# Optimization experiments

Hardware: AMD Instinct MI355X
Metric: run time of the kernel (lower is better)

Reference implementation:

```python
import jax, jax.numpy as jnp
import numpy as np

H = 16          # nhead
N_LAYERS = 4    # stacks (weights are SHARED across stacks, as in the torch module)
PAD_IDX = 1
EPS = 1e-6
NEG = -1e9


def _pos_encoding(S, d):
    den = jnp.exp(-jnp.arange(0, d, 2, dtype=jnp.float32) * (np.log(10000.0) / d))
    ang = jnp.arange(S, dtype=jnp.float32)[:, None] * den[None, :]  # (S, d/2)
    pe = jnp.zeros((S, d), jnp.float32)
    pe = pe.at[:, 0::2].set(jnp.sin(ang)).at[:, 1::2].set(jnp.cos(ang))
    return pe


def _layer_norm(x, g, b):
    mu = jnp.mean(x, axis=-1, keepdims=True)
    var = jnp.mean((x - mu) ** 2, axis=-1, keepdims=True)
    return (x - mu) * jax.lax.rsqrt(var + EPS) * g + b


def _split_heads(x):
    B, S, d = x.shape
    return x.reshape(B, S, H, d // H).transpose(0, 2, 1, 3)  # (B,H,S,dk)


def _mha(q_in, k_in, v_in, mask, wq, bq, wk, bk, wv, bv, wo, bo):
    q = _split_heads(q_in @ wq + bq)
    k = _split_heads(k_in @ wk + bk)
    v = _split_heads(v_in @ wv + bv)
    dk = v.shape[-1]
    score = jnp.einsum('bhqd,bhkd->bhqk', q, k) / jnp.sqrt(jnp.float32(dk))
    if mask is not None:
        score = jnp.where(mask, score, NEG)
    p = jax.nn.softmax(score, axis=-1)
    out = jnp.einsum('bhqk,bhkd->bhqd', p, v)
    B, _, S, _ = out.shape
    out = out.transpose(0, 2, 1, 3).reshape(B, S, H * dk)
    return out @ wo + bo


def setup_inputs() -> dict:
    key = jax.random.key(0)
    B, St, Sm, d, dff, V = 4, 1024, 1024, 1024, 4096, 32000
    ks = jax.random.split(key, 32)
    sc = 1.0 / np.sqrt(d)
    inp = {
        'target_result': jax.random.randint(ks[0], (B, St), 0, V),
        'memory': jax.random.normal(ks[1], (B, Sm, d), jnp.float32),
        'emb': jax.random.normal(ks[2], (V, d), jnp.float32) * sc,
        'ff_w1': jax.random.normal(ks[3], (d, dff), jnp.float32) * sc,
        'ff_b1': jnp.zeros((dff,), jnp.float32),
        'ff_w2': jax.random.normal(ks[4], (dff, d), jnp.float32) / np.sqrt(dff),
        'ff_b2': jnp.zeros((d,), jnp.float32),
        'ln_g': jnp.ones((d,), jnp.float32),
        'ln_b': jnp.zeros((d,), jnp.float32),
    }
    i = 5
    for pre in ('sa', 'xa'):
        for nm in ('q', 'k', 'v', 'o'):
            inp[f'{pre}_w{nm}'] = jax.random.normal(ks[i], (d, d), jnp.float32) * sc
            inp[f'{pre}_b{nm}'] = jnp.zeros((d,), jnp.float32)
            i += 1
    return inp


def reference(target_result, memory, emb,
              sa_wq, sa_bq, sa_wk, sa_bk, sa_wv, sa_bv, sa_wo, sa_bo,
              xa_wq, xa_bq, xa_wk, xa_bk, xa_wv, xa_bv, xa_wo, xa_bo,
              ff_w1, ff_b1, ff_w2, ff_b2, ln_g, ln_b):
    B, St = target_result.shape
    d = emb.shape[1]
    # embed + scale + positional encoding (dropout = eval/identity)
    x = emb[target_result] * jnp.sqrt(jnp.float32(d)) + _pos_encoding(St, d)[None]
    # masks: pad mask (B,1,St,1) & causal (St,St) -> (B,1,St,St); source mask all-ones -> None
    pad = (target_result != PAD_IDX)[:, None, :, None]
    causal = jnp.tril(jnp.ones((St, St), bool))[None, None]
    tgt_mask = pad & causal
    out = x
    for _ in range(N_LAYERS):
        n = _layer_norm(out, ln_g, ln_b)
        out = out + _mha(n, n, n, tgt_mask,
                         sa_wq, sa_bq, sa_wk, sa_bk, sa_wv, sa_bv, sa_wo, sa_bo)
        n = _layer_norm(out, ln_g, ln_b)
        out = out + _mha(n, memory, memory, None,
                         xa_wq, xa_bq, xa_wk, xa_bk, xa_wv, xa_bv, xa_wo, xa_bo)
        n = _layer_norm(out, ln_g, ln_b)
        out = out + (jax.nn.relu(n @ ff_w1 + ff_b1) @ ff_w2 + ff_b2)
    return _layer_norm(out, ln_g, ln_b)
```

## Files before the change

### kernel.cpp

```cpp
#include <hip/hip_runtime.h>

typedef unsigned short u16;
typedef unsigned int u32;
typedef float f32x4 __attribute__((ext_vector_type(4)));
typedef float f32x16 __attribute__((ext_vector_type(16)));
typedef __bf16 bf16x8 __attribute__((ext_vector_type(8)));
typedef short short8 __attribute__((ext_vector_type(8)));
typedef u32 u32x4 __attribute__((ext_vector_type(4)));

#define DINLINE static __device__ __forceinline__

DINLINE u16 f2bf(float f) {
  u32 u = __builtin_bit_cast(u32, f);
  u += 0x7fffu + ((u >> 16) & 1u);
  return (u16)(u >> 16);
}

DINLINE float b2f(u32 lo16) {
  u32 u = lo16 << 16;
  return __builtin_bit_cast(float, u);
}

DINLINE f32x4 mfma16(short8 a, short8 b, f32x4 c) {
  return __builtin_amdgcn_mfma_f32_16x16x32_bf16(
      __builtin_bit_cast(bf16x8, a), __builtin_bit_cast(bf16x8, b), c, 0, 0, 0);
}

DINLINE f32x16 mfma32(short8 a, short8 b, f32x16 c) {
  return __builtin_amdgcn_mfma_f32_32x32x16_bf16(
      __builtin_bit_cast(bf16x8, a), __builtin_bit_cast(bf16x8, b), c, 0, 0, 0);
}

DINLINE u32 cvtpk(float lo, float hi) {
  u32 r;
  asm("v_cvt_pk_bf16_f32 %0, %1, %2" : "=v"(r) : "v"(lo), "v"(hi));
  return r;
}

DINLINE void plswap(u32& a, u32& b) {
  auto r = __builtin_amdgcn_permlane32_swap(a, b, false, false);
  a = (u32)r[0];
  b = (u32)r[1];
}

DINLINE void gld16(const void* g, void* l) {
  __builtin_amdgcn_global_load_lds(
      (const __attribute__((address_space(1))) void*)g,
      (__attribute__((address_space(3))) void*)l, 16, 0, 0);
}

struct W8 {
  const float* src[8];
  u16* dst[8];
  float scale[8];
};
__global__ __launch_bounds__(256) void transpose_wt8(W8 p) {
  __shared__ float tile[32][33];
  const int z = blockIdx.z;
  const float* __restrict__ src = p.src[z];
  u16* __restrict__ dst = p.dst[z];
  const float scale = p.scale[z];
  int n0 = blockIdx.x * 32, k0 = blockIdx.y * 32;
  int tx = threadIdx.x, ty = threadIdx.y;
#pragma unroll
  for (int j = 0; j < 32; j += 8)
    tile[ty + j][tx] = src[(size_t)(k0 + ty + j) * 1024 + n0 + tx];
  __syncthreads();
#pragma unroll
  for (int j = 0; j < 32; j += 8)
    dst[(size_t)(n0 + ty + j) * 1024 + k0 + tx] = f2bf(tile[tx][ty + j] * scale);
}

__global__ __launch_bounds__(256) void transpose_wt(const float* __restrict__ src,
                                                    u16* __restrict__ dst, int K, int N,
                                                    float scale) {
  __shared__ float tile[32][33];
  int n0 = blockIdx.x * 32, k0 = blockIdx.y * 32;
  int tx = threadIdx.x, ty = threadIdx.y;
#pragma unroll
  for (int j = 0; j < 32; j += 8)
    tile[ty + j][tx] = src[(size_t)(k0 + ty + j) * N + n0 + tx];
  __syncthreads();
#pragma unroll
  for (int j = 0; j < 32; j += 8)
    dst[(size_t)(n0 + ty + j) * K + k0 + tx] = f2bf(tile[tx][ty + j] * scale);
}

__global__ __launch_bounds__(256) void cvt_bf16(const float* __restrict__ src,
                                                u16* __restrict__ dst) {
  size_t i = (size_t)blockIdx.x * 256 + threadIdx.x;
  float4 v = ((const float4*)src)[i];
  u32 lo = (u32)f2bf(v.x) | ((u32)f2bf(v.y) << 16);
  u32 hi = (u32)f2bf(v.z) | ((u32)f2bf(v.w) << 16);
  uint2 o; o.x = lo; o.y = hi;
  ((uint2*)dst)[i] = o;
}

__global__ void prep_bias(const float* __restrict__ a, const float* __restrict__ b,
                          const float* __restrict__ c, const float* __restrict__ xq,
                          float* __restrict__ oqkv, float* __restrict__ oxq, float sa) {
  int i = blockIdx.x * 256 + threadIdx.x;
  if (i < 1024) oqkv[i] = a[i] * sa;
  else if (i < 2048) oqkv[i] = b[i - 1024];
  else if (i < 3072) oqkv[i] = c[i - 2048];
  else oxq[i - 3072] = xq[i - 3072] * sa;
}

__global__ __launch_bounds__(256) void pe_k(float* __restrict__ pe) {
  int s = blockIdx.x;
  for (int c = threadIdx.x; c < 1024; c += 256) {
    int i = c >> 1;
    float den = expf(-(float)(2 * i) * 0.0089944739960705f);
    float ang = (float)s * den;
    pe[s * 1024 + c] = (c & 1) ? cosf(ang) : sinf(ang);
  }
}

__global__ __launch_bounds__(256) void embed_pe(const int* __restrict__ tgt,
                                                const float* __restrict__ emb,
                                                const float* __restrict__ pe,
                                                float* __restrict__ x,
                                                u16* __restrict__ xbf) {
  int row = blockIdx.x;
  int s = row & 1023;
  int tok = tgt[row];
  float4 e = ((const float4*)(emb + (size_t)tok * 1024))[threadIdx.x];
  float4 p = ((const float4*)(pe + (size_t)s * 1024))[threadIdx.x];
  float4 o;
  o.x = e.x * 32.0f + p.x; o.y = e.y * 32.0f + p.y;
  o.z = e.z * 32.0f + p.z; o.w = e.w * 32.0f + p.w;
  ((float4*)(x + (size_t)row * 1024))[threadIdx.x] = o;
  ushort4 ob;
  ob.x = f2bf(o.x); ob.y = f2bf(o.y); ob.z = f2bf(o.z); ob.w = f2bf(o.w);
  ((ushort4*)(xbf + (size_t)row * 1024))[threadIdx.x] = ob;
}

template <int MODE>
__global__ __launch_bounds__(256) void ln2_k(const float* __restrict__ Xf,
                                             const u16* __restrict__ Xb,
                                             const float* __restrict__ g,
                                             const float* __restrict__ bta,
                                             u16* __restrict__ obf,
                                             float* __restrict__ of) {
  const int t = threadIdx.x;
  const int row = blockIdx.x * 2 + (t >> 7);
  const int c = t & 127;
  float v[8];
  if (MODE == 1) {
    float4 a = ((const float4*)(Xf + (size_t)row * 1024))[c * 2];
    float4 b4 = ((const float4*)(Xf + (size_t)row * 1024))[c * 2 + 1];
    v[0] = a.x; v[1] = a.y; v[2] = a.z; v[3] = a.w;
    v[4] = b4.x; v[5] = b4.y; v[6] = b4.z; v[7] = b4.w;
  } else {
    u32x4 p = *(const u32x4*)(Xb + (size_t)row * 1024 + c * 8);
#pragma unroll
    for (int i = 0; i < 4; ++i) {
      v[2 * i] = b2f(p[i]);
      v[2 * i + 1] = b2f(p[i] >> 16);
    }
  }
  float s = 0.f, sq = 0.f;
#pragma unroll
  for (int i = 0; i < 8; ++i) { s += v[i]; sq += v[i] * v[i]; }
#pragma unroll
  for (int o = 1; o < 64; o <<= 1) {
    s += __shfl_xor(s, o);
    sq += __shfl_xor(sq, o);
  }
  __shared__ float red[8];
  const int wid = t >> 6;
  if ((t & 63) == 0) { red[wid * 2] = s; red[wid * 2 + 1] = sq; }
  __syncthreads();
  const int base = (t >> 7) * 4;
  s = red[base] + red[base + 2];
  sq = red[base + 1] + red[base + 3];
  float mean = s * (1.0f / 1024.0f);
  float var = sq * (1.0f / 1024.0f) - mean * mean;
  float rstd = rsqrtf(var + 1e-6f);
  float4 g0 = ((const float4*)g)[c * 2], g1 = ((const float4*)g)[c * 2 + 1];
  float4 b0 = ((const float4*)bta)[c * 2], b1 = ((const float4*)bta)[c * 2 + 1];
  float gv[8] = {g0.x, g0.y, g0.z, g0.w, g1.x, g1.y, g1.z, g1.w};
  float bv[8] = {b0.x, b0.y, b0.z, b0.w, b1.x, b1.y, b1.z, b1.w};
  float y[8];
#pragma unroll
  for (int i = 0; i < 8; ++i) y[i] = (v[i] - mean) * rstd * gv[i] + bv[i];
  if (MODE == 1) {
    float4 o0, o1;
    o0.x = y[0]; o0.y = y[1]; o0.z = y[2]; o0.w = y[3];
    o1.x = y[4]; o1.y = y[5]; o1.z = y[6]; o1.w = y[7];
    ((float4*)(of + (size_t)row * 1024))[c * 2] = o0;
    ((float4*)(of + (size_t)row * 1024))[c * 2 + 1] = o1;
  } else {
    u32x4 o;
#pragma unroll
    for (int i = 0; i < 4; ++i)
      o[i] = (u32)f2bf(y[2 * i]) | ((u32)f2bf(y[2 * i + 1]) << 16);
    *(u32x4*)(obf + (size_t)row * 1024 + c * 8) = o;
  }
}

template <int BM, int EPI>
__global__ __launch_bounds__(256) void gemm2c(
    const u16* __restrict__ A, const u16* __restrict__ Bt,
    const float* __restrict__ bias, float* __restrict__ X,
    u16* __restrict__ Cbf, int N, int K) {
  constexpr int ABYT = BM * 128;
  constexpr int BBYT = 128 * 128;
  constexpr int BUF = ABYT + BBYT;
  constexpr int MF = BM / 32;
  __shared__ __align__(16) char smem[3 * BUF];

  const int tid = threadIdx.x;
  const int w = tid >> 6, l = tid & 63;
  const int lg = l >> 4, lc = l & 15;
  const int nwg = gridDim.x * gridDim.y;
  int bid = blockIdx.y * gridDim.x + blockIdx.x;
  bid = (bid & 7) * (nwg >> 3) + (bid >> 3);
  const int m0 = (bid / gridDim.x) * BM, n0 = (bid % gridDim.x) * 128;
  const int wr = w >> 1, wc = w & 1;
  const char* Ab = (const char*)A;
  const char* Bb = (const char*)Bt;
  const size_t sA = (size_t)K * 2;

  f32x4 acc[MF][4];
  const f32x4 zv = {0.f, 0.f, 0.f, 0.f};
#pragma unroll
  for (int m = 0; m < MF; ++m)
#pragma unroll
    for (int n = 0; n < 4; ++n) acc[m][n] = zv;

  const int srow = l >> 3;
  const int scol = ((l & 7) ^ srow) << 4;

  auto stage = [&](char* buf, int kt) {
    const size_t kb = (size_t)kt << 7;
#pragma unroll
    for (int i = 0; i < BM / 32; ++i) {
      const int r = i * 32 + w * 8 + srow;
      gld16(Ab + (size_t)(m0 + r) * sA + kb + scol, buf + (i * 4 + w) * 1024 + l * 16);
    }
#pragma unroll
    for (int i = 0; i < 4; ++i) {
      const int r = i * 32 + w * 8 + srow;
      gld16(Bb + (size_t)(n0 + r) * sA + kb + scol,
            buf + ABYT + (i * 4 + w) * 1024 + l * 16);
    }
  };

  char* p0 = smem;
  char* p1 = smem + BUF;
  char* p2 = smem + 2 * BUF;

  stage(p0, 0);
  stage(p1, 1);
  __builtin_amdgcn_sched_barrier(0);
  asm volatile("s_waitcnt vmcnt(6)" ::: "memory");
  __builtin_amdgcn_s_barrier();
  __builtin_amdgcn_sched_barrier(0);

  const int nkt = K >> 6;
  for (int kt = 0; kt < nkt; ++kt) {
    if (kt + 2 < nkt) stage(p2, kt + 2);
    const char* As = p0;
    const char* Bs = p0 + ABYT;
    __builtin_amdgcn_s_setprio(1);
#pragma unroll
    for (int ks = 0; ks < 2; ++ks) {
      short8 af[MF], bf4[4];
#pragma unroll
      for (int m = 0; m < MF; ++m) {
        int row = wr * (BM / 2) + m * 16 + lc;
        int col = (ks * 64 + (lg << 4)) ^ ((row & 7) << 4);
        af[m] = *(const short8*)(As + row * 128 + col);
      }
#pragma unroll
      for (int n = 0; n < 4; ++n) {
        int row = wc * 64 + n * 16 + lc;
        int col = (ks * 64 + (lg << 4)) ^ ((row & 7) << 4);
        bf4[n] = *(const short8*)(Bs + row * 128 + col);
      }
#pragma unroll
      for (int m = 0; m < MF; ++m)
#pragma unroll
        for (int n = 0; n < 4; ++n) acc[m][n] = mfma16(af[m], bf4[n], acc[m][n]);
    }
    __builtin_amdgcn_s_setprio(0);
    __builtin_amdgcn_sched_barrier(0);
    if (kt + 2 < nkt) {
      asm volatile("s_waitcnt vmcnt(6) lgkmcnt(0)" ::: "memory");
    } else {
      asm volatile("s_waitcnt vmcnt(0) lgkmcnt(0)" ::: "memory");
    }
    __builtin_amdgcn_s_barrier();
    __builtin_amdgcn_sched_barrier(0);
    char* t = p0; p0 = p1; p1 = p2; p2 = t;
  }

  float bv[4];
#pragma unroll
  for (int n = 0; n < 4; ++n) bv[n] = bias[n0 + wc * 64 + n * 16 + lc];

  if (EPI <= 1) {
    u16* ct = (u16*)smem;
#pragma unroll
    for (int m = 0; m < MF; ++m)
#pragma unroll
      for (int n = 0; n < 4; ++n)
#pragma unroll
        for (int r = 0; r < 4; ++r) {
          int row = wr * (BM / 2) + m * 16 + (lg << 2) + r;
          int col = wc * 64 + n * 16 + lc;
          float v = acc[m][n][r] + bv[n];
          if (EPI == 1) v = v > 0.f ? v : 0.f;
          ct[row * 136 + col] = f2bf(v);
        }
    __syncthreads();
#pragma unroll
    for (int j = 0; j < BM / 16; ++j) {
      int c = j * 256 + tid;
      int row = c >> 4, colb = (c & 15) * 8;
      *(short8*)(Cbf + (size_t)(m0 + row) * N + n0 + colb) =
          *(const short8*)(ct + row * 136 + colb);
    }
  } else if (EPI == 2) {
    float* cf = (float*)smem;
#pragma unroll
    for (int m = 0; m < MF; ++m)
#pragma unroll
      for (int n = 0; n < 4; ++n)
#pragma unroll
        for (int r = 0; r < 4; ++r) {
          int row = wr * (BM / 2) + m * 16 + (lg << 2) + r;
          int col = wc * 64 + n * 16 + lc;
          cf[row * 128 + col] = acc[m][n][r] + bv[n];
        }
    __syncthreads();
#pragma unroll
    for (int j = 0; j < BM / 8; ++j) {
      int c = j * 256 + tid;
      int row = c >> 5, colb = (c & 31) * 4;
      size_t idx = (size_t)(m0 + row) * N + n0 + colb;
      float4 s4 = *(const float4*)(cf + row * 128 + colb);
      float4 xv = *(const float4*)(X + idx);
      xv.x += s4.x; xv.y += s4.y; xv.z += s4.z; xv.w += s4.w;
      *(float4*)(X + idx) = xv;
      ushort4 ob;
      ob.x = f2bf(xv.x); ob.y = f2bf(xv.y); ob.z = f2bf(xv.z); ob.w = f2bf(xv.w);
      *(ushort4*)(Cbf + idx) = ob;
    }
  } else {
    u16* ct = (u16*)smem;
#pragma unroll
    for (int m = 0; m < MF; ++m)
#pragma unroll
      for (int n = 0; n < 4; ++n)
#pragma unroll
        for (int r = 0; r < 4; ++r) {
          int row = wr * (BM / 2) + m * 16 + (lg << 2) + r;
          int col = wc * 64 + n * 16 + lc;
          ct[col * 136 + row] = f2bf(acc[m][n][r] + bv[n]);
        }
    __syncthreads();
    const int bb = m0 >> 10, ms = m0 & 1023;
#pragma unroll
    for (int j = 0; j < BM / 16; ++j) {
      int flat = j * 256 + tid;
      int sb = flat & (BM / 8 - 1);
      int col = flat / (BM / 8);
      int n = n0 + col;
      u16* dst = Cbf + (size_t)(((bb << 4) + (n >> 6)) * 64 + (n & 63)) * 1024 + ms + sb * 8;
      *(short8*)dst = *(const short8*)(ct + col * 136 + sb * 8);
    }
  }
}

template <int EPI>
__global__ __launch_bounds__(512) void gemm3b(
    const u16* __restrict__ A, const u16* __restrict__ Bt,
    const float* __restrict__ bias, u16* __restrict__ Cbf, int N, int K) {
  constexpr int ABYT = 32768;
  constexpr int BBYT = 32768;
  __shared__ __align__(16) char smem[2 * (ABYT + BBYT)];

  const int tid = threadIdx.x;
  const int w = tid >> 6, l = tid & 63;
  const int lg = l >> 4, lc = l & 15;
  const int nwg = gridDim.x * gridDim.y;
  int bid = blockIdx.y * gridDim.x + blockIdx.x;
  bid = (bid & 7) * (nwg >> 3) + (bid >> 3);
  const int m0 = (bid / gridDim.x) * 256, n0 = (bid % gridDim.x) * 256;
  const int wr = w >> 2, wc = w & 3;
  const char* Ab = (const char*)A;
  const char* Bb = (const char*)Bt;
  const size_t sA = (size_t)K * 2;

  f32x4 acc[8][4];
  const f32x4 zv = {0.f, 0.f, 0.f, 0.f};
#pragma unroll
  for (int m = 0; m < 8; ++m)
#pragma unroll
    for (int n = 0; n < 4; ++n) acc[m][n] = zv;

  const int srow = l >> 3;
  const int scol = ((l & 7) ^ srow) << 4;

  auto stage = [&](char* buf, int kt) {
    const size_t kb = (size_t)kt << 7;
#pragma unroll
    for (int i = 0; i < 4; ++i) {
      const int r = i * 64 + w * 8 + srow;
      gld16(Ab + (size_t)(m0 + r) * sA + kb + scol, buf + (i * 8 + w) * 1024 + l * 16);
    }
#pragma unroll
    for (int i = 0; i < 4; ++i) {
      const int r = i * 64 + w * 8 + srow;
      gld16(Bb + (size_t)(n0 + r) * sA + kb + scol,
            buf + ABYT + (i * 8 + w) * 1024 + l * 16);
    }
  };

  stage(smem, 0);
  __syncthreads();

  const int nkt = K >> 6;
  int cur = 0;
  for (int kt = 0; kt < nkt; ++kt) {
    char* As = smem + cur * (ABYT + BBYT);
    char* Bs = As + ABYT;
    if (kt + 1 < nkt) stage(smem + (cur ^ 1) * (ABYT + BBYT), kt + 1);
    __builtin_amdgcn_s_setprio(1);
#pragma unroll
    for (int ks = 0; ks < 2; ++ks) {
      short8 bf4[4];
#pragma unroll
      for (int n = 0; n < 4; ++n) {
        int row = wc * 64 + n * 16 + lc;
        int col = (ks * 64 + (lg << 4)) ^ ((row & 7) << 4);
        bf4[n] = *(const short8*)(Bs + row * 128 + col);
      }
#pragma unroll
      for (int m = 0; m < 8; ++m) {
        int row = wr * 128 + m * 16 + lc;
        int col = (ks * 64 + (lg << 4)) ^ ((row & 7) << 4);
        short8 af = *(const short8*)(As + row * 128 + col);
#pragma unroll
        for (int n = 0; n < 4; ++n) acc[m][n] = mfma16(af, bf4[n], acc[m][n]);
      }
    }
    __builtin_amdgcn_s_setprio(0);
    __syncthreads();
    cur ^= 1;
  }

  float bv[4];
#pragma unroll
  for (int n = 0; n < 4; ++n) bv[n] = bias[n0 + wc * 64 + n * 16 + lc];
  u16* ct = (u16*)smem;
#pragma unroll
  for (int h = 0; h < 2; ++h) {
    __syncthreads();
    if (wr == h) {
#pragma unroll
      for (int m = 0; m < 8; ++m)
#pragma unroll
        for (int n = 0; n < 4; ++n)
#pragma unroll
          for (int r = 0; r < 4; ++r) {
            int row = m * 16 + (lg << 2) + r;
            int col = wc * 64 + n * 16 + lc;
            float v = acc[m][n][r] + bv[n];
            if (EPI == 1) v = v > 0.f ? v : 0.f;
            ct[row * 264 + col] = f2bf(v);
          }
    }
    __syncthreads();
#pragma unroll
    for (int j = 0; j < 8; ++j) {
      int c = j * 512 + tid;
      int row = c >> 5, colb = (c & 31) * 8;
      *(short8*)(Cbf + (size_t)(m0 + h * 128 + row) * N + n0 + colb) =
          *(const short8*)(ct + row * 264 + colb);
    }
  }
}

__global__ __launch_bounds__(512) void gemm3q(
    const u16* __restrict__ A, const u16* __restrict__ Bt,
    const float* __restrict__ bias, u16* __restrict__ Cqk, u16* __restrict__ Vt, int K) {
  constexpr int ABYT = 32768;
  constexpr int BBYT = 32768;
  __shared__ __align__(16) char smem[2 * (ABYT + BBYT)];

  const int tid = threadIdx.x;
  const int w = tid >> 6, l = tid & 63;
  const int lg = l >> 4, lc = l & 15;
  const int nwg = gridDim.x * gridDim.y;
  int bid = blockIdx.y * gridDim.x + blockIdx.x;
  bid = (bid & 7) * (nwg >> 3) + (bid >> 3);
  const int m0 = (bid / gridDim.x) * 256, n0 = (bid % gridDim.x) * 256;
  const int wr = w >> 2, wc = w & 3;
  const char* Ab = (const char*)A;
  const char* Bb = (const char*)Bt;
  const size_t sA = (size_t)K * 2;

  f32x4 acc[8][4];
  const f32x4 zv = {0.f, 0.f, 0.f, 0.f};
#pragma unroll
  for (int m = 0; m < 8; ++m)
#pragma unroll
    for (int n = 0; n < 4; ++n) acc[m][n] = zv;

  const int srow = l >> 3;
  const int scol = ((l & 7) ^ srow) << 4;

  auto stage = [&](char* buf, int kt) {
    const size_t kb = (size_t)kt << 7;
#pragma unroll
    for (int i = 0; i < 4; ++i) {
      const int r = i * 64 + w * 8 + srow;
      gld16(Ab + (size_t)(m0 + r) * sA + kb + scol, buf + (i * 8 + w) * 1024 + l * 16);
    }
#pragma unroll
    for (int i = 0; i < 4; ++i) {
      const int r = i * 64 + w * 8 + srow;
      gld16(Bb + (size_t)(n0 + r) * sA + kb + scol,
            buf + ABYT + (i * 8 + w) * 1024 + l * 16);
    }
  };

  stage(smem, 0);
  __syncthreads();

  const int nkt = K >> 6;
  int cur = 0;
  for (int kt = 0; kt < nkt; ++kt) {
    char* As = smem + cur * (ABYT + BBYT);
    char* Bs = As + ABYT;
    if (kt + 1 < nkt) stage(smem + (cur ^ 1) * (ABYT + BBYT), kt + 1);
    __builtin_amdgcn_s_setprio(1);
#pragma unroll
    for (int ks = 0; ks < 2; ++ks) {
      short8 bf4[4];
#pragma unroll
      for (int n = 0; n < 4; ++n) {
        int row = wc * 64 + n * 16 + lc;
        int col = (ks * 64 + (lg << 4)) ^ ((row & 7) << 4);
        bf4[n] = *(const short8*)(Bs + row * 128 + col);
      }
#pragma unroll
      for (int m = 0; m < 8; ++m) {
        int row = wr * 128 + m * 16 + lc;
        int col = (ks * 64 + (lg << 4)) ^ ((row & 7) << 4);
        short8 af = *(const short8*)(As + row * 128 + col);
#pragma unroll
        for (int n = 0; n < 4; ++n) acc[m][n] = mfma16(af, bf4[n], acc[m][n]);
      }
    }
    __builtin_amdgcn_s_setprio(0);
    __syncthreads();
    cur ^= 1;
  }

  float bv[4];
#pragma unroll
  for (int n = 0; n < 4; ++n) bv[n] = bias[n0 + wc * 64 + n * 16 + lc];
  u16* ct = (u16*)smem;

  if (n0 < 2048) {
#pragma unroll
    for (int h = 0; h < 2; ++h) {
      __syncthreads();
      if (wr == h) {
#pragma unroll
        for (int m = 0; m < 8; ++m)
#pragma unroll
          for (int n = 0; n < 4; ++n)
#pragma unroll
            for (int r = 0; r < 4; ++r) {
              int row = m * 16 + (lg << 2) + r;
              int col = wc * 64 + n * 16 + lc;
              ct[row * 264 + col] = f2bf(acc[m][n][r] + bv[n]);
            }
      }
      __syncthreads();
#pragma unroll
      for (int j = 0; j < 8; ++j) {
        int c = j * 512 + tid;
        int row = c >> 5, colb = (c & 31) * 8;
        *(short8*)(Cqk + (size_t)(m0 + h * 128 + row) * 2048 + n0 + colb) =
            *(const short8*)(ct + row * 264 + colb);
      }
    }
  } else {
    const int bb = m0 >> 10, ms = m0 & 1023;
#pragma unroll
    for (int h = 0; h < 2; ++h) {
      __syncthreads();
      if (wr == h) {
#pragma unroll
        for (int m = 0; m < 8; ++m)
#pragma unroll
          for (int n = 0; n < 4; ++n)
#pragma unroll
            for (int r = 0; r < 4; ++r) {
              int row = m * 16 + (lg << 2) + r;
              int col = wc * 64 + n * 16 + lc;
              ct[col * 136 + row] = f2bf(acc[m][n][r] + bv[n]);
            }
      }
      __syncthreads();
#pragma unroll
      for (int j = 0; j < 8; ++j) {
        int flat = j * 512 + tid;
        int col = flat >> 4, sb = flat & 15;
        int n = n0 + col - 2048;
        u16* dst = Vt + (size_t)(((bb << 4) + (n >> 6)) * 64 + (n & 63)) * 1024 +
                   ms + h * 128 + sb * 8;
        *(short8*)dst = *(const short8*)(ct + col * 136 + sb * 8);
      }
    }
  }
}

template <bool CAUSAL>
__global__ __launch_bounds__(512) void attn_lds(
    const u16* __restrict__ Qp, int sQ, const u16* __restrict__ Kp, int sK,
    const u16* __restrict__ Vt, const int* __restrict__ tgt,
    u16* __restrict__ Out) {
  __shared__ __align__(16) char smem[2][32768];
  const int tid = threadIdx.x;
  const int w = tid >> 6, l = tid & 63;
  const int bh = blockIdx.x & 63;
  const int p = blockIdx.x >> 6;
  const int qt = CAUSAL ? ((w < 4) ? (p * 4 + w) : (31 - (p * 4 + (w - 4))))
                        : (p * 8 + w);
  const int b = bh >> 4, h = bh & 15;
  const int lq = l & 31, hi = l >> 5;
  const int q0 = qt * 32;

  const char* Kc = (const char*)(Kp + (size_t)b * 1024 * sK + h * 64);
  const char* Vc = (const char*)(Vt + (size_t)bh * 64 * 1024);
  const u16* Qh = Qp + (size_t)b * 1024 * sQ + h * 64;

  short8 qb[4];
  {
    const u16* qrow = Qh + (size_t)(q0 + lq) * sQ + hi * 8;
#pragma unroll
    for (int c = 0; c < 4; ++c) qb[c] = *(const short8*)(qrow + c * 16);
  }

  bool row_ok = true;
  int my_nkt = 16;
  int blk_nst = CAUSAL ? (8 - p) : 8;
  if (CAUSAL) {
    row_ok = (tgt[b * 1024 + q0 + lq] != 1);
    bool anypad_w = __any(!row_ok);
    __shared__ int s_pad;
    if (tid == 0) s_pad = 0;
    __syncthreads();
    if (anypad_w && l == 0) s_pad = 1;
    __syncthreads();
    if (s_pad) { my_nkt = 16; blk_nst = 8; }
    else my_nkt = (qt >> 1) + 1;
  }

  const int srow = l >> 3;
  const int scol = ((l & 7) ^ srow) << 4;
  auto stage = [&](int buf, int st) {
    const int k0 = st * 128;
    char* Ks = smem[buf];
    char* Vs = smem[buf] + 16384;
    const int r = w * 8 + srow;
#pragma unroll
    for (int t2 = 0; t2 < 2; ++t2) {
      gld16(Kc + (size_t)(k0 + t2 * 64 + r) * sK * 2 + scol, Ks + t2 * 8192 + r * 128);
      gld16(Vc + (size_t)r * 2048 + (size_t)(k0 + t2 * 64) * 2 + scol,
            Vs + t2 * 8192 + r * 128);
    }
  };

  float m = -3.0e38f, lsum = 0.f;
  f32x16 oacc[2];
#pragma unroll
  for (int r = 0; r < 16; ++r) { oacc[0][r] = 0.f; oacc[1][r] = 0.f; }

  stage(0, 0);
  __syncthreads();
  int cur = 0;

  for (int st = 0; st < blk_nst; ++st) {
    if (st + 1 < blk_nst) stage(cur ^ 1, st + 1);
#pragma unroll
    for (int t2 = 0; t2 < 2; ++t2) {
      const int t64 = st * 2 + t2;
      if (t64 < my_nkt) {
        const char* Ks = smem[cur] + t2 * 8192;
        const char* Vs = smem[cur] + 16384 + t2 * 8192;
        const int k0 = t64 * 64;
        f32x16 stt[2];
        __builtin_amdgcn_s_setprio(1);
#pragma unroll
        for (int s = 0; s < 2; ++s) {
          const int row = s * 32 + lq;
          const int swz = (row & 7) << 4;
          f32x16 a;
#pragma unroll
          for (int r = 0; r < 16; ++r) a[r] = 0.f;
#pragma unroll
          for (int c = 0; c < 4; ++c) {
            short8 kb = *(const short8*)(Ks + row * 128 + ((c * 32 + hi * 16) ^ swz));
            a = mfma32(kb, qb[c], a);
          }
          stt[s] = a;
        }
        __builtin_amdgcn_s_setprio(0);
        if (CAUSAL) {
#pragma unroll
          for (int s = 0; s < 2; ++s) {
            if (!row_ok || (k0 + s * 32 + 31 > q0)) {
#pragma unroll
              for (int r = 0; r < 16; ++r) {
                int kg = k0 + s * 32 + (r & 3) + 8 * (r >> 2) + 4 * hi;
                bool ok = row_ok && (kg <= q0 + lq);
                if (!ok) stt[s][r] = -1e9f;
              }
            }
          }
        }
        float tm;
        {
          float v[16];
#pragma unroll
          for (int r = 0; r < 16; ++r) v[r] = fmaxf(stt[0][r], stt[1][r]);
#pragma unroll
          for (int w2 = 8; w2 >= 1; w2 >>= 1)
#pragma unroll
            for (int r = 0; r < w2; ++r) v[r] = fmaxf(v[r], v[r + w2]);
          tm = v[0];
        }
        tm = fmaxf(tm, __shfl_xor(tm, 32));
        if (!__all(tm <= m + 8.0f)) {
          float mn = fmaxf(m, tm);
          float alpha = __expf(m - mn);
          lsum *= alpha;
          m = mn;
#pragma unroll
          for (int r = 0; r < 16; ++r) {
            int crow = (r & 3) + 8 * (r >> 2) + 4 * hi;
            float av = __shfl(alpha, crow);
            oacc[0][r] *= av;
            oacc[1][r] *= av;
          }
        }
        float tsa0 = 0.f, tsa1 = 0.f, tsa2 = 0.f, tsa3 = 0.f;
#pragma unroll
        for (int s = 0; s < 2; ++s) {
#pragma unroll
          for (int r = 0; r < 16; ++r) {
            float e = __expf(stt[s][r] - m);
            stt[s][r] = e;
            if ((r & 3) == 0) tsa0 += e;
            else if ((r & 3) == 1) tsa1 += e;
            else if ((r & 3) == 2) tsa2 += e;
            else tsa3 += e;
          }
        }
        float ts = (tsa0 + tsa1) + (tsa2 + tsa3);
        ts += __shfl_xor(ts, 32);
        lsum += ts;
        short8 pa[4];
#pragma unroll
        for (int s = 0; s < 2; ++s) {
          u32 cc[8];
#pragma unroll
          for (int t = 0; t < 4; ++t) {
            cc[2 * t]     = cvtpk(stt[s][4 * t + 0], stt[s][4 * t + 1]);
            cc[2 * t + 1] = cvtpk(stt[s][4 * t + 2], stt[s][4 * t + 3]);
          }
          plswap(cc[0], cc[2]);
          plswap(cc[1], cc[3]);
          plswap(cc[4], cc[6]);
          plswap(cc[5], cc[7]);
          u32x4 w0 = {cc[0], cc[1], cc[2], cc[3]};
          u32x4 w1 = {cc[4], cc[5], cc[6], cc[7]};
          pa[2 * s]     = __builtin_bit_cast(short8, w0);
          pa[2 * s + 1] = __builtin_bit_cast(short8, w1);
        }
        __builtin_amdgcn_s_setprio(1);
#pragma unroll
        for (int dt = 0; dt < 2; ++dt) {
          const int row = dt * 32 + lq;
          const int swz = (row & 7) << 4;
#pragma unroll
          for (int c = 0; c < 4; ++c) {
            short8 vb = *(const short8*)(Vs + row * 128 + ((c * 32 + hi * 16) ^ swz));
            oacc[dt] = mfma32(pa[c], vb, oacc[dt]);
          }
        }
        __builtin_amdgcn_s_setprio(0);
      }
    }
    __syncthreads();
    cur ^= 1;
  }

#pragma unroll
  for (int r = 0; r < 16; ++r) {
    int crow = (r & 3) + 8 * (r >> 2) + 4 * hi;
    float lv = __shfl(lsum, crow);
    float linv = 1.0f / lv;
    int qg = q0 + crow;
    size_t base = ((size_t)b * 1024 + qg) * 1024 + h * 64 + lq;
    Out[base] = f2bf(oacc[0][r] * linv);
    Out[base + 32] = f2bf(oacc[1][r] * linv);
  }
}

extern "C" void kernel_launch(void* const* d_in, const int* in_sizes, int n_in,
                              void* d_out, int out_size, void* d_ws, size_t ws_size,
                              hipStream_t stream) {
  const int* tgt = (const int*)d_in[0];
  const float* memory = (const float*)d_in[1];
  const float* emb = (const float*)d_in[2];
  const float* ff_w1 = (const float*)d_in[3];
  const float* ff_b1 = (const float*)d_in[4];
  const float* ff_w2 = (const float*)d_in[5];
  const float* ff_b2 = (const float*)d_in[6];
  const float* ln_g = (const float*)d_in[7];
  const float* ln_b = (const float*)d_in[8];
  const float* sa_wq = (const float*)d_in[9];
  const float* sa_bq = (const float*)d_in[10];
  const float* sa_wk = (const float*)d_in[11];
  const float* sa_bk = (const float*)d_in[12];
  const float* sa_wv = (const float*)d_in[13];
  const float* sa_bv = (const float*)d_in[14];
  const float* sa_wo = (const float*)d_in[15];
  const float* sa_bo = (const float*)d_in[16];
  const float* xa_wq = (const float*)d_in[17];
  const float* xa_bq = (const float*)d_in[18];
  const float* xa_wk = (const float*)d_in[19];
  const float* xa_bk = (const float*)d_in[20];
  const float* xa_wv = (const float*)d_in[21];
  const float* xa_bv = (const float*)d_in[22];
  const float* xa_wo = (const float*)d_in[23];
  const float* xa_bo = (const float*)d_in[24];

  char* ws = (char*)d_ws;
  size_t off = 0;
  auto alloc = [&](size_t bytes) {
    char* p = ws + off;
    off += (bytes + 255) & ~(size_t)255;
    return p;
  };
  float* x   = (float*)alloc(4096ull * 1024 * 4);
  u16* xbf   = (u16*)alloc(4096ull * 1024 * 2);
  u16* nbf   = (u16*)alloc(4096ull * 1024 * 2);
  u16* qkv   = (u16*)alloc(4096ull * 2048 * 2);
  u16* q2    = (u16*)alloc(4096ull * 1024 * 2);
  u16* attn  = (u16*)alloc(4096ull * 1024 * 2);
  u16* vt    = (u16*)alloc(64ull * 64 * 1024 * 2);
  u16* kx    = (u16*)alloc(4096ull * 1024 * 2);
  u16* vtx   = (u16*)alloc(64ull * 64 * 1024 * 2);
  u16* h1    = (u16*)alloc(4096ull * 4096 * 2);
  u16* memb  = (u16*)alloc(4096ull * 1024 * 2);
  u16* w_qkv = (u16*)alloc(3072ull * 1024 * 2);
  u16* w_sao = (u16*)alloc(1024ull * 1024 * 2);
  u16* w_xaq = (u16*)alloc(1024ull * 1024 * 2);
  u16* w_xak = (u16*)alloc(1024ull * 1024 * 2);
  u16* w_xav = (u16*)alloc(1024ull * 1024 * 2);
  u16* w_xao = (u16*)alloc(1024ull * 1024 * 2);
  u16* w_ff1 = (u16*)alloc(4096ull * 1024 * 2);
  u16* w_ff2 = (u16*)alloc(1024ull * 4096 * 2);
  float* b_qkv = (float*)alloc(3072 * 4);
  float* b_xaq = (float*)alloc(1024 * 4);
  float* pe    = (float*)alloc(1024ull * 1024 * 4);

  dim3 blk(256);
  dim3 b32(32, 8);
  const float QS = 0.125f;

  W8 wp;
  wp.src[0] = sa_wq; wp.dst[0] = w_qkv;               wp.scale[0] = QS;
  wp.src[1] = sa_wk; wp.dst[1] = w_qkv + 1024 * 1024; wp.scale[1] = 1.f;
  wp.src[2] = sa_wv; wp.dst[2] = w_qkv + 2048 * 1024; wp.scale[2] = 1.f;
  wp.src[3] = sa_wo; wp.dst[3] = w_sao;               wp.scale[3] = 1.f;
  wp.src[4] = xa_wq; wp.dst[4] = w_xaq;               wp.scale[4] = QS;
  wp.src[5] = xa_wk; wp.dst[5] = w_xak;               wp.scale[5] = 1.f;
  wp.src[6] = xa_wv; wp.dst[6] = w_xav;               wp.scale[6] = 1.f;
  wp.src[7] = xa_wo; wp.dst[7] = w_xao;               wp.scale[7] = 1.f;
  transpose_wt8<<<dim3(32, 32, 8), b32, 0, stream>>>(wp);
  transpose_wt<<<dim3(128, 32), b32, 0, stream>>>(ff_w1, w_ff1, 1024, 4096, 1.f);
  transpose_wt<<<dim3(32, 128), b32, 0, stream>>>(ff_w2, w_ff2, 4096, 1024, 1.f);
  prep_bias<<<16, blk, 0, stream>>>(sa_bq, sa_bk, sa_bv, xa_bq, b_qkv, b_xaq, QS);
  cvt_bf16<<<4096, blk, 0, stream>>>(memory, memb);
  pe_k<<<1024, blk, 0, stream>>>(pe);
  embed_pe<<<4096, blk, 0, stream>>>(tgt, emb, pe, x, xbf);

  gemm2c<64, 0><<<dim3(8, 64), blk, 0, stream>>>(memb, w_xak, xa_bk, nullptr, kx, 1024, 1024);
  gemm2c<64, 3><<<dim3(8, 64), blk, 0, stream>>>(memb, w_xav, xa_bv, nullptr, vtx, 1024, 1024);

  for (int layer = 0; layer < 4; ++layer) {
    ln2_k<2><<<2048, blk, 0, stream>>>(nullptr, xbf, ln_g, ln_b, nbf, nullptr);
    gemm3q<<<dim3(12, 16), dim3(512), 0, stream>>>(nbf, w_qkv, b_qkv, qkv, vt, 1024);
    attn_lds<true><<<256, dim3(512), 0, stream>>>(qkv, 2048, qkv + 1024, 2048, vt, tgt, attn);
    gemm2c<64, 2><<<dim3(8, 64), blk, 0, stream>>>(attn, w_sao, sa_bo, x, xbf, 1024, 1024);
    ln2_k<2><<<2048, blk, 0, stream>>>(nullptr, xbf, ln_g, ln_b, nbf, nullptr);
    gemm2c<64, 0><<<dim3(8, 64), blk, 0, stream>>>(nbf, w_xaq, b_xaq, nullptr, q2, 1024, 1024);
    attn_lds<false><<<256, dim3(512), 0, stream>>>(q2, 1024, kx, 1024, vtx, nullptr, attn);
    gemm2c<64, 2><<<dim3(8, 64), blk, 0, stream>>>(attn, w_xao, xa_bo, x, xbf, 1024, 1024);
    ln2_k<2><<<2048, blk, 0, stream>>>(nullptr, xbf, ln_g, ln_b, nbf, nullptr);
    gemm3b<1><<<dim3(16, 16), dim3(512), 0, stream>>>(nbf, w_ff1, ff_b1, h1, 4096, 1024);
    gemm2c<64, 2><<<dim3(8, 64), blk, 0, stream>>>(h1, w_ff2, ff_b2, x, xbf, 1024, 4096);
  }
  ln2_k<1><<<2048, blk, 0, stream>>>(x, nullptr, ln_g, ln_b, nullptr, (float*)d_out);
}
```

Before: 1.040 ms.

## Process two query tiles per wave in attention to reuse K/V fragments

Each attention block now uses 256 threads (4 waves) instead of 512, and every wave handles two 32-row query tiles (paired causally as qA and 31-qA). The K and V fragments read from LDS are shared across both tiles, so LDS reads per MFMA drop by half, and each thread stages twice as many rows. The cost is doubled accumulator and score registers per wave and launch_bounds(256,2), which may raise register pressure and reduce the number of waves available to hide latency.

```diff
diff --git a/kernel.cpp b/kernel.cpp
--- a/kernel.cpp
+++ b/kernel.cpp
@@ -623,7 +623,7 @@
 }
 
 template <bool CAUSAL>
-__global__ __launch_bounds__(512) void attn_lds(
+__global__ __launch_bounds__(256, 2) void attn_q2(
     const u16* __restrict__ Qp, int sQ, const u16* __restrict__ Kp, int sK,
     const u16* __restrict__ Vt, const int* __restrict__ tgt,
     u16* __restrict__ Out) {
@@ -632,36 +632,42 @@
   const int w = tid >> 6, l = tid & 63;
   const int bh = blockIdx.x & 63;
   const int p = blockIdx.x >> 6;
-  const int qt = CAUSAL ? ((w < 4) ? (p * 4 + w) : (31 - (p * 4 + (w - 4))))
-                        : (p * 8 + w);
   const int b = bh >> 4, h = bh & 15;
   const int lq = l & 31, hi = l >> 5;
-  const int q0 = qt * 32;
+
+  const int qA = p * 4 + w;
+  const int qB = CAUSAL ? (31 - qA) : (16 + qA);
+  const int q0A = qA * 32, q0B = qB * 32;
 
   const char* Kc = (const char*)(Kp + (size_t)b * 1024 * sK + h * 64);
   const char* Vc = (const char*)(Vt + (size_t)bh * 64 * 1024);
   const u16* Qh = Qp + (size_t)b * 1024 * sQ + h * 64;
 
-  short8 qb[4];
+  short8 qbA[4], qbB[4];
   {
-    const u16* qrow = Qh + (size_t)(q0 + lq) * sQ + hi * 8;
-#pragma unroll
-    for (int c = 0; c < 4; ++c) qb[c] = *(const short8*)(qrow + c * 16);
-  }
-
-  bool row_ok = true;
-  int my_nkt = 16;
+    const u16* qrA = Qh + (size_t)(q0A + lq) * sQ + hi * 8;
+    const u16* qrB = Qh + (size_t)(q0B + lq) * sQ + hi * 8;
+#pragma unroll
+    for (int c = 0; c < 4; ++c) {
+      qbA[c] = *(const short8*)(qrA + c * 16);
+      qbB[c] = *(const short8*)(qrB + c * 16);
+    }
+  }
+
+  bool rokA = true, rokB = true;
+  int nktA = 16, nktB = 16;
   int blk_nst = CAUSAL ? (8 - p) : 8;
   if (CAUSAL) {
-    row_ok = (tgt[b * 1024 + q0 + lq] != 1);
-    bool anypad_w = __any(!row_ok);
+    rokA = (tgt[b * 1024 + q0A + lq] != 1);
+    rokB = (tgt[b * 1024 + q0B + lq] != 1);
+    bool anypad_w = __any(!rokA || !rokB);
     __shared__ int s_pad;
     if (tid == 0) s_pad = 0;
     __syncthreads();
     if (anypad_w && l == 0) s_pad = 1;
     __syncthreads();
-    if (s_pad) { my_nkt = 16; blk_nst = 8; }
-    else my_nkt = (qt >> 1) + 1;
+    if (s_pad) { nktA = 16; nktB = 16; blk_nst = 8; }
+    else { nktA = (qA >> 1) + 1; nktB = (qB >> 1) + 1; }
   }
 
   const int srow = l >> 3;
@@ -670,19 +676,100 @@
     const int k0 = st * 128;
     char* Ks = smem[buf];
     char* Vs = smem[buf] + 16384;
-    const int r = w * 8 + srow;
-#pragma unroll
-    for (int t2 = 0; t2 < 2; ++t2) {
-      gld16(Kc + (size_t)(k0 + t2 * 64 + r) * sK * 2 + scol, Ks + t2 * 8192 + r * 128);
-      gld16(Vc + (size_t)r * 2048 + (size_t)(k0 + t2 * 64) * 2 + scol,
-            Vs + t2 * 8192 + r * 128);
+#pragma unroll
+    for (int g = 0; g < 2; ++g) {
+      const int r = w * 16 + g * 8 + srow;
+#pragma unroll
+      for (int t2 = 0; t2 < 2; ++t2) {
+        gld16(Kc + (size_t)(k0 + t2 * 64 + r) * sK * 2 + scol, Ks + t2 * 8192 + r * 128);
+        gld16(Vc + (size_t)r * 2048 + (size_t)(k0 + t2 * 64) * 2 + scol,
+              Vs + t2 * 8192 + r * 128);
+      }
     }
   };
 
-  float m = -3.0e38f, lsum = 0.f;
-  f32x16 oacc[2];
-#pragma unroll
-  for (int r = 0; r < 16; ++r) { oacc[0][r] = 0.f; oacc[1][r] = 0.f; }
+  float mA = -3.0e38f, lsA = 0.f, mB = -3.0e38f, lsB = 0.f;
+  f32x16 oaccA[2], oaccB[2];
+#pragma unroll
+  for (int r = 0; r < 16; ++r) {
+    oaccA[0][r] = 0.f; oaccA[1][r] = 0.f;
+    oaccB[0][r] = 0.f; oaccB[1][r] = 0.f;
+  }
+
+  auto dotile = [&](f32x16 (&stt)[2], float& m_, float& ls_, f32x16 (&oacc_)[2],
+                    short8 (&pa_)[4], int q0_, bool rok_, int k0) {
+    if (CAUSAL) {
+#pragma unroll
+      for (int s = 0; s < 2; ++s) {
+        if (!rok_ || (k0 + s * 32 + 31 > q0_)) {
+#pragma unroll
+          for (int r = 0; r < 16; ++r) {
+            int kg = k0 + s * 32 + (r & 3) + 8 * (r >> 2) + 4 * hi;
+            bool ok = rok_ && (kg <= q0_ + lq);
+            if (!ok) stt[s][r] = -1e9f;
+          }
+        }
+      }
+    }
+    float tm;
+    {
+      float v[16];
+#pragma unroll
+      for (int r = 0; r < 16; ++r) v[r] = fmaxf(stt[0][r], stt[1][r]);
+#pragma unroll
+      for (int w2 = 8; w2 >= 1; w2 >>= 1)
+#pragma unroll
+        for (int r = 0; r < w2; ++r) v[r] = fmaxf(v[r], v[r + w2]);
+      tm = v[0];
+    }
+    tm = fmaxf(tm, __shfl_xor(tm, 32));
+    if (!__all(tm <= m_ + 8.0f)) {
+      float mn = fmaxf(m_, tm);
+      float alpha = __expf(m_ - mn);
+      ls_ *= alpha;
+      m_ = mn;
+#pragma unroll
+      for (int r = 0; r < 16; ++r) {
+        int crow = (r & 3) + 8 * (r >> 2) + 4 * hi;
+        float av = __shfl(alpha, crow);
+        oacc_[0][r] *= av;
+        oacc_[1][r] *= av;
+      }
+    }
+    float t0 = 0.f, t1 = 0.f, t2s = 0.f, t3 = 0.f;
+#pragma unroll
+    for (int s = 0; s < 2; ++s) {
+#pragma unroll
+      for (int r = 0; r < 16; ++r) {
+        float e = __expf(stt[s][r] - m_);
+        stt[s][r] = e;
+        if ((r & 3) == 0) t0 += e;
+        else if ((r & 3) == 1) t1 += e;
+        else if ((r & 3) == 2) t2s += e;
+        else t3 += e;
+      }
+    }
+    float ts = (t0 + t1) + (t2s + t3);
+    ts += __shfl_xor(ts, 32);
+    ls_ += ts;
+#pragma unroll
+    for (int s = 0; s < 2; ++s) {
+      u32 cc[8];
+#pragma unroll
+      for (int t = 0; t < 4; ++t) {
+        cc[2 * t]     = cvtpk(stt[s][4 * t + 0], stt[s][4 * t + 1]);
+        cc[2 * t + 1] = cvtpk(stt[s][4 * t + 2], stt[s][4 * t + 3]);
+      }
+      plswap(cc[0], cc[2]);
+      plswap(cc[1], cc[3]);
+      plswap(cc[4], cc[6]);
+      plswap(cc[5], cc[7]);
+      u32x4 w0 = {cc[0], cc[1], cc[2], cc[3]};
+      u32x4 w1 = {cc[4], cc[5], cc[6], cc[7]};
+      pa_[2 * s]     = __builtin_bit_cast(short8, w0);
+      pa_[2 * s + 1] = __builtin_bit_cast(short8, w1);
+    }
+  };
 
   stage(0, 0);
   __syncthreads();
@@ -693,99 +780,34 @@
 #pragma unroll
     for (int t2 = 0; t2 < 2; ++t2) {
       const int t64 = st * 2 + t2;
-      if (t64 < my_nkt) {
+      const bool actA = t64 < nktA;
+      const bool actB = t64 < nktB;
+      if (actA || actB) {
         const char* Ks = smem[cur] + t2 * 8192;
         const char* Vs = smem[cur] + 16384 + t2 * 8192;
         const int k0 = t64 * 64;
-        f32x16 stt[2];
+        f32x16 sA2[2], sB2[2];
         __builtin_amdgcn_s_setprio(1);
 #pragma unroll
         for (int s = 0; s < 2; ++s) {
           const int row = s * 32 + lq;
           const int swz = (row & 7) << 4;
-          f32x16 a;
-#pragma unroll
-          for (int r = 0; r < 16; ++r) a[r] = 0.f;
+          f32x16 a0, a1;
+#pragma unroll
+          for (int r = 0; r < 16; ++r) { a0[r] = 0.f; a1[r] = 0.f; }
 #pragma unroll
           for (int c = 0; c < 4; ++c) {
             short8 kb = *(const short8*)(Ks + row * 128 + ((c * 32 + hi * 16) ^ swz));
-            a = mfma32(kb, qb[c], a);
+            if (actA) a0 = mfma32(kb, qbA[c], a0);
+            if (actB) a1 = mfma32(kb, qbB[c], a1);
           }
-          stt[s] = a;
+          sA2[s] = a0;
+          sB2[s] = a1;
         }
         __builtin_amdgcn_s_setprio(0);
-        if (CAUSAL) {
-#pragma unroll
-          for (int s = 0; s < 2; ++s) {
-            if (!row_ok || (k0 + s * 32 + 31 > q0)) {
-#pragma unroll
-              for (int r = 0; r < 16; ++r) {
-                int kg = k0 + s * 32 + (r & 3) + 8 * (r >> 2) + 4 * hi;
-                bool ok = row_ok && (kg <= q0 + lq);
-                if (!ok) stt[s][r] = -1e9f;
-              }
-            }
-          }
-        }
-        float tm;
-        {
-          float v[16];
-#pragma unroll
-          for (int r = 0; r < 16; ++r) v[r] = fmaxf(stt[0][r], stt[1][r]);
-#pragma unroll
-          for (int w2 = 8; w2 >= 1; w2 >>= 1)
-#pragma unroll
-            for (int r = 0; r < w2; ++r) v[r] = fmaxf(v[r], v[r + w2]);
-          tm = v[0];
-        }
-        tm = fmaxf(tm, __shfl_xor(tm, 32));
-        if (!__all(tm <= m + 8.0f)) {
-          float mn = fmaxf(m, tm);
-          float alpha = __expf(m - mn);
-          lsum *= alpha;
-          m = mn;
-#pragma unroll
-          for (int r = 0; r < 16; ++r) {
-            int crow = (r & 3) + 8 * (r >> 2) + 4 * hi;
-            float av = __shfl(alpha, crow);
-            oacc[0][r] *= av;
-            oacc[1][r] *= av;
-          }
-        }
-        float tsa0 = 0.f, tsa1 = 0.f, tsa2 = 0.f, tsa3 = 0.f;
-#pragma unroll
-        for (int s = 0; s < 2; ++s) {
-#pragma unroll
-          for (int r = 0; r < 16; ++r) {
-            float e = __expf(stt[s][r] - m);
-            stt[s][r] = e;
-            if ((r & 3) == 0) tsa0 += e;
-            else if ((r & 3) == 1) tsa1 += e;
-            else if ((r & 3) == 2) tsa2 += e;
-            else tsa3 += e;
-          }
-        }
-        float ts = (tsa0 + tsa1) + (tsa2 + tsa3);
-        ts += __shfl_xor(ts, 32);
-        lsum += ts;
-        short8 pa[4];
-#pragma unroll
-        for (int s = 0; s < 2; ++s) {
-          u32 cc[8];
-#pragma unroll
-          for (int t = 0; t < 4; ++t) {
-            cc[2 * t]     = cvtpk(stt[s][4 * t + 0], stt[s][4 * t + 1]);
-            cc[2 * t + 1] = cvtpk(stt[s][4 * t + 2], stt[s][4 * t + 3]);
-          }
-          plswap(cc[0], cc[2]);
-          plswap(cc[1], cc[3]);
-          plswap(cc[4], cc[6]);
-          plswap(cc[5], cc[7]);
-          u32x4 w0 = {cc[0], cc[1], cc[2], cc[3]};
-          u32x4 w1 = {cc[4], cc[5], cc[6], cc[7]};
-          pa[2 * s]     = __builtin_bit_cast(short8, w0);
-          pa[2 * s + 1] = __builtin_bit_cast(short8, w1);
-        }
+        short8 paA[4], paB[4];
+        if (actA) dotile(sA2, mA, lsA, oaccA, paA, q0A, rokA, k0);
+        if (actB) dotile(sB2, mB, lsB, oaccB, paB, q0B, rokB, k0);
         __builtin_amdgcn_s_setprio(1);
 #pragma unroll
         for (int dt = 0; dt < 2; ++dt) {
@@ -794,7 +816,8 @@
 #pragma unroll
           for (int c = 0; c < 4; ++c) {
             short8 vb = *(const short8*)(Vs + row * 128 + ((c * 32 + hi * 16) ^ swz));
-            oacc[dt] = mfma32(pa[c], vb, oacc[dt]);
+            if (actA) oaccA[dt] = mfma32(paA[c], vb, oaccA[dt]);
+            if (actB) oaccB[dt] = mfma32(paB[c], vb, oaccB[dt]);
           }
         }
         __builtin_amdgcn_s_setprio(0);
@@ -807,12 +830,16 @@
 #pragma unroll
   for (int r = 0; r < 16; ++r) {
     int crow = (r & 3) + 8 * (r >> 2) + 4 * hi;
-    float lv = __shfl(lsum, crow);
-    float linv = 1.0f / lv;
-    int qg = q0 + crow;
-    size_t base = ((size_t)b * 1024 + qg) * 1024 + h * 64 + lq;
-    Out[base] = f2bf(oacc[0][r] * linv);
-    Out[base + 32] = f2bf(oacc[1][r] * linv);
+    float lvA = __shfl(lsA, crow);
+    float lvB = __shfl(lsB, crow);
+    float liA = 1.0f / lvA;
+    float liB = 1.0f / lvB;
+    size_t baseA = ((size_t)b * 1024 + q0A + crow) * 1024 + h * 64 + lq;
+    size_t baseB = ((size_t)b * 1024 + q0B + crow) * 1024 + h * 64 + lq;
+    Out[baseA] = f2bf(oaccA[0][r] * liA);
+    Out[baseA + 32] = f2bf(oaccA[1][r] * liA);
+    Out[baseB] = f2bf(oaccB[0][r] * liB);
+    Out[baseB + 32] = f2bf(oaccB[1][r] * liB);
   }
 }
 
@@ -902,11 +929,11 @@
   for (int layer = 0; layer < 4; ++layer) {
     ln2_k<2><<<2048, blk, 0, stream>>>(nullptr, xbf, ln_g, ln_b, nbf, nullptr);
     gemm3q<<<dim3(12, 16), dim3(512), 0, stream>>>(nbf, w_qkv, b_qkv, qkv, vt, 1024);
-    attn_lds<true><<<256, dim3(512), 0, stream>>>(qkv, 2048, qkv + 1024, 2048, vt, tgt, attn);
+    attn_q2<true><<<256, blk, 0, stream>>>(qkv, 2048, qkv + 1024, 2048, vt, tgt, attn);
     gemm2c<64, 2><<<dim3(8, 64), blk, 0, stream>>>(attn, w_sao, sa_bo, x, xbf, 1024, 1024);
     ln2_k<2><<<2048, blk, 0, stream>>>(nullptr, xbf, ln_g, ln_b, nbf, nullptr);
     gemm2c<64, 0><<<dim3(8, 64), blk, 0, stream>>>(nbf, w_xaq, b_xaq, nullptr, q2, 1024, 1024);
-    attn_lds<false><<<256, dim3(512), 0, stream>>>(q2, 1024, kx, 1024, vtx, nullptr, attn);
+    attn_q2<false><<<256, blk, 0, stream>>>(q2, 1024, kx, 1024, vtx, nullptr, attn);
     gemm2c<64, 2><<<dim3(8, 64), blk, 0, stream>>>(attn, w_xao, xa_bo, x, xbf, 1024, 1024);
     ln2_k<2><<<2048, blk, 0, stream>>>(nullptr, xbf, ln_g, ln_b, nbf, nullptr);
     gemm3b<1><<<dim3(16, 16), dim3(512), 0, stream>>>(nbf, w_ff1, ff_b1, h1, 4096, 1024);
```

After: 1.211 ms. 1.17x slower.
